# Kernel optimization log

Hardware: AMD Instinct MI355X
Metric: run time of the kernel (lower is better)

Reference implementation:

```python
import jax, jax.numpy as jnp
import numpy as np

N = 131072        # total nodes (2048 graphs * MAX_N)
E = 1048576       # edges
F_IN = 128        # g_feature_n
INT_D = 256       # int_d
H1, C1 = 8, 8     # gl: heads, head_d
C2 = 256          # gl2: out channels, heads=1
MAX_N = 64
NEG_SLOPE = 0.2
BN_EPS = 1e-5


def _gat_conv(x, src, dst, W, att_src, att_dst, bias, heads, out_c):
    """PyG GATConv (concat=True), self-loops already appended to src/dst."""
    n = x.shape[0]
    h = (x @ W.T).reshape(n, heads, out_c)                  # [N,H,C]
    a_s = jnp.sum(h * att_src, axis=-1)                     # [N,H]
    a_d = jnp.sum(h * att_dst, axis=-1)                     # [N,H]
    alpha = jax.nn.leaky_relu(a_s[src] + a_d[dst], NEG_SLOPE)  # [E',H]
    amax = jax.ops.segment_max(alpha, dst, num_segments=n)  # stable segment softmax
    e = jnp.exp(alpha - amax[dst])
    denom = jax.ops.segment_sum(e, dst, num_segments=n)
    w = e / (denom[dst] + 1e-16)                            # [E',H]
    out = jax.ops.segment_sum(h[src] * w[..., None], dst, num_segments=n)
    return out.reshape(n, heads * out_c) + bias


def setup_inputs() -> dict:
    key = jax.random.key(0)
    ks = jax.random.split(key, 20)
    s = 0.1
    return {
        "x": jax.random.normal(ks[0], (N, F_IN), jnp.float32),
        "edge_index": jax.random.randint(ks[1], (2, E), 0, N, jnp.int64),
        # lin_embed
        "We": jax.random.normal(ks[2], (INT_D, F_IN), jnp.float32) * s,
        "be": jnp.zeros((INT_D,), jnp.float32),
        # batchnorm (eval mode, running stats)
        "bn_gamma": jnp.ones((INT_D,), jnp.float32),
        "bn_beta": jnp.zeros((INT_D,), jnp.float32),
        "bn_mean": jax.random.normal(ks[3], (INT_D,), jnp.float32) * 0.01,
        "bn_var": jax.random.uniform(ks[4], (INT_D,), jnp.float32, 0.5, 1.5),
        # gl: GATConv(INT_D -> C1, heads=H1)
        "W1": jax.random.normal(ks[5], (H1 * C1, INT_D), jnp.float32) * s,
        "as1": jax.random.normal(ks[6], (1, H1, C1), jnp.float32) * s,
        "ad1": jax.random.normal(ks[7], (1, H1, C1), jnp.float32) * s,
        "b1": jnp.zeros((H1 * C1,), jnp.float32),
        # gl2: GATConv(H1*C1 -> C2, heads=1)
        "W2": jax.random.normal(ks[8], (C2, H1 * C1), jnp.float32) * s,
        "as2": jax.random.normal(ks[9], (1, 1, C2), jnp.float32) * s,
        "ad2": jax.random.normal(ks[10], (1, 1, C2), jnp.float32) * s,
        "b2": jnp.zeros((C2,), jnp.float32),
        # lin_out
        "Wo": jax.random.normal(ks[11], (1, INT_D), jnp.float32) * s,
        "bo": jnp.zeros((1,), jnp.float32),
    }


def reference(x, edge_index, We, be, bn_gamma, bn_beta, bn_mean, bn_var,
              W1, as1, ad1, b1, W2, as2, ad2, b2, Wo, bo):
    n = x.shape[0]
    loops = jnp.arange(n)
    src = jnp.concatenate([edge_index[0], loops])  # add_self_loops=True (PyG default)
    dst = jnp.concatenate([edge_index[1], loops])

    h = x @ We.T + be
    h = (h - bn_mean) * jax.lax.rsqrt(bn_var + BN_EPS) * bn_gamma + bn_beta

    h = jax.nn.elu(_gat_conv(h, src, dst, W1, as1, ad1, b1, H1, C1))
    h = _gat_conv(h, src, dst, W2, as2, ad2, b2, 1, C2)

    mu = (h @ Wo.T + bo).reshape(-1, MAX_N, 1)
    return mu, jnp.zeros_like(mu)
```

## Files before the change

### kernel.cpp

```cpp
#include <hip/hip_runtime.h>
#include <hip/hip_bf16.h>

#define NN 131072
#define NE 1048576
#define INVLN2 1.44269504088896341f

typedef unsigned short u16;
typedef unsigned int u32;

__device__ __forceinline__ float bf2f(u16 u) {
  return __uint_as_float(((unsigned int)u) << 16);
}
__device__ __forceinline__ u16 f2bf(float f) {
  unsigned int u = __float_as_uint(f);
  unsigned int r = ((u >> 16) & 1u) + 0x7fffu;
  return (u16)((u + r) >> 16);
}
__device__ __forceinline__ float leakyf(float x) { return x >= 0.f ? x : 0.2f * x; }

constexpr size_t OFF_H1   = 0;
constexpr size_t OFF_AS1N = 16777216;
constexpr size_t OFF_AD1N = 20971520;
constexpr size_t OFF_ZS   = 25165824;
constexpr size_t OFF_AD2N = 26214400;
constexpr size_t OFF_RP   = 26738688;
constexpr size_t OFF_WOFF = 27264000;
constexpr size_t OFF_COL  = 27788288;
constexpr size_t OFF_MP   = 31982592;
constexpr size_t OFF_C1AC = 32023552;
constexpr size_t OFF_V2   = 32023840;
constexpr size_t OFF_BSUM = 32024624;

__global__ __launch_bounds__(1024) void scanA_kernel(const int* cnt, int* rp, int* bsum) {
  __shared__ int buf[1024];
  int t = threadIdx.x;
  int i = blockIdx.x * 1024 + t;
  int v = cnt[i];
  buf[t] = v;
  __syncthreads();
  for (int off = 1; off < 1024; off <<= 1) {
    int a = (t >= off) ? buf[t - off] : 0;
    __syncthreads();
    buf[t] += a;
    __syncthreads();
  }
  rp[i] = buf[t] - v;
  if (t == 1023) bsum[blockIdx.x] = buf[t];
}
__global__ void scanB_kernel(int* bsum, int* rp) {
  __shared__ int buf[128];
  int t = threadIdx.x;
  int v = bsum[t];
  buf[t] = v;
  __syncthreads();
  for (int off = 1; off < 128; off <<= 1) {
    int a = (t >= off) ? buf[t - off] : 0;
    __syncthreads();
    buf[t] += a;
    __syncthreads();
  }
  bsum[t] = buf[t] - v;
  if (t == 127) rp[NN] = buf[127];
}
__global__ __launch_bounds__(1024) void scanC_kernel(int* rp, const int* bsum, int* wo) {
  int i = blockIdx.x * 1024 + threadIdx.x;
  int v = rp[i] + bsum[blockIdx.x];
  rp[i] = v;
  wo[i] = v;
}

__global__ __launch_bounds__(256) void count_fold_kernel(
    const int* __restrict__ ei, int* cnt, const float* W1, const float* We,
    const float* be, const float* bng, const float* bnb, const float* bnm,
    const float* bnv, const float* as1, const float* ad1, const float* W2,
    const float* as2, const float* ad2, const float* Wo, const float* b2,
    const float* bo, float* MP, float* c1ac, float* v2) {
  int b = blockIdx.x;
  int t = threadIdx.x;
  if (b < 4096) {
    int p = b & 7;
    int base = (b >> 3) * 2048;
    int dsts[8];
#pragma unroll
    for (int j = 0; j < 8; ++j) dsts[j] = ei[NE + base + t + 256 * j];
#pragma unroll
    for (int j = 0; j < 8; ++j)
      if ((dsts[j] >> 14) == p) atomicAdd(&cnt[dsts[j]], 1);
  } else if (b < 4136) {
    __shared__ float L[2][256];
    int mrow = b - 4096;
    int r0 = mrow * 2;
    int lr = t >> 7, k = t & 127;
    float sgc = bng[t] * rsqrtf(bnv[t] + 1e-5f);
#pragma unroll
    for (int q = 0; q < 2; ++q) {
      int r = r0 + q;
      float coef;
      if (r < 64) {
        coef = W1[r * 256 + t];
      } else if (r < 72) {
        int h = r - 64;
        coef = 0.f;
#pragma unroll
        for (int j = 0; j < 8; ++j) coef += as1[h * 8 + j] * W1[(h * 8 + j) * 256 + t];
        coef *= INVLN2;
      } else {
        int h = r - 72;
        coef = 0.f;
#pragma unroll
        for (int j = 0; j < 8; ++j) coef += ad1[h * 8 + j] * W1[(h * 8 + j) * 256 + t];
        coef *= INVLN2;
      }
      L[q][t] = coef * sgc;
    }
    __syncthreads();
    float acc = 0.f;
    for (int c = 0; c < 256; ++c) acc += L[lr][c] * We[c * 128 + k];
    MP[(size_t)(r0 + lr) * 128 + k] = acc;
  } else if (b == 4136) {
    __shared__ float ofs[256];
    __shared__ float c1l[64];
    float sgc = bng[t] * rsqrtf(bnv[t] + 1e-5f);
    ofs[t] = (be[t] - bnm[t]) * sgc + bnb[t];
    __syncthreads();
    if (t < 64) {
      float a = 0.f;
      for (int c = 0; c < 256; ++c) a += W1[t * 256 + c] * ofs[c];
      c1ac[t] = a;
      c1l[t] = a;
    }
    __syncthreads();
    if (t < 8) {
      float s = 0.f;
#pragma unroll
      for (int j = 0; j < 8; ++j) s += c1l[t * 8 + j] * (as1[t * 8 + j] + ad1[t * 8 + j]);
      c1ac[64 + t] = s * INVLN2;
    }
  } else {
    __shared__ float pa[4][64], pd[4][64], pz[4][64];
    int k = t & 63, part = t >> 6;
    float a = 0.f, d = 0.f, z = 0.f;
    for (int c = part * 64; c < part * 64 + 64; ++c) {
      float w = W2[c * 64 + k];
      a += as2[c] * w;
      d += ad2[c] * w;
      z += Wo[c] * w;
    }
    pa[part][k] = a;
    pd[part][k] = d;
    pz[part][k] = z;
    __syncthreads();
    if (t < 64) {
      v2[t]       = (pa[0][t] + pa[1][t] + pa[2][t] + pa[3][t]) * INVLN2;
      v2[64 + t]  = (pd[0][t] + pd[1][t] + pd[2][t] + pd[3][t]) * INVLN2;
      v2[128 + t] = pz[0][t] + pz[1][t] + pz[2][t] + pz[3][t];
      float cc = b2[t] * Wo[t] + b2[64 + t] * Wo[64 + t] +
                 b2[128 + t] * Wo[128 + t] + b2[192 + t] * Wo[192 + t];
      for (int o = 1; o < 64; o <<= 1) cc += __shfl_xor(cc, o);
      if (t == 0) v2[192] = cc + bo[0];
    }
  }
}

__global__ __launch_bounds__(256) void fill_gemm_kernel(const float* __restrict__ x,
                                                        const float* __restrict__ MP,
                                                        u16* __restrict__ h1,
                                                        float* __restrict__ as1n,
                                                        float* __restrict__ ad1n,
                                                        const int* __restrict__ ei,
                                                        int* wo, int* colv) {
  __shared__ float4 sM[80 * 32];
  int b = blockIdx.x;
  int t = threadIdx.x;
  if (b >= 512) {
    int fb = b - 512;
    int p = fb & 7;
    int base = (fb >> 3) * 2048;
    int dsts[8], srcs[8];
#pragma unroll
    for (int j = 0; j < 8; ++j) {
      dsts[j] = ei[NE + base + t + 256 * j];
      srcs[j] = ei[base + t + 256 * j];
    }
#pragma unroll
    for (int j = 0; j < 8; ++j) {
      if ((dsts[j] >> 14) == p) {
        int pos = atomicAdd(&wo[dsts[j]], 1);
        colv[pos] = srcs[j];
      }
    }
    return;
  }
  int lane = t & 63, wv = t >> 6;
  const float4* MPv = (const float4*)MP;
  for (int i = t; i < 2560; i += 256) sM[i] = MPv[i];
  __syncthreads();
  int c0 = (wv & 1) * 40;
  size_t r0 = (size_t)b * 256 + (wv >> 1) * 128 + lane;
  const float4* x0 = (const float4*)(x + r0 * 128);
  const float4* x1 = (const float4*)(x + (r0 + 64) * 128);
  float a0[40], a1[40];
#pragma unroll
  for (int c = 0; c < 40; ++c) { a0[c] = 0.f; a1[c] = 0.f; }
  for (int q = 0; q < 32; ++q) {
    float4 cx0 = x0[q];
    float4 cx1 = x1[q];
    const float4* mp = sM + c0 * 32 + q;
#pragma unroll
    for (int c = 0; c < 40; ++c) {
      float4 B = mp[c * 32];
      a0[c] += cx0.x * B.x; a0[c] += cx0.y * B.y;
      a0[c] += cx0.z * B.z; a0[c] += cx0.w * B.w;
      a1[c] += cx1.x * B.x; a1[c] += cx1.y * B.y;
      a1[c] += cx1.z * B.z; a1[c] += cx1.w * B.w;
    }
  }
#pragma unroll
  for (int rr = 0; rr < 2; ++rr) {
    size_t row = r0 + rr * 64;
    if (c0 == 0) {
      u32 ux[20];
#pragma unroll
      for (int j = 0; j < 20; ++j) {
        float lo = rr ? a1[2 * j] : a0[2 * j];
        float hi = rr ? a1[2 * j + 1] : a0[2 * j + 1];
        ux[j] = (u32)f2bf(lo) | ((u32)f2bf(hi) << 16);
      }
      uint4* dst = (uint4*)(h1 + row * 64);
#pragma unroll
      for (int j = 0; j < 5; ++j)
        dst[j] = make_uint4(ux[4 * j], ux[4 * j + 1], ux[4 * j + 2], ux[4 * j + 3]);
    } else {
      u32 ux[12];
#pragma unroll
      for (int j = 0; j < 12; ++j) {
        float lo = rr ? a1[2 * j] : a0[2 * j];
        float hi = rr ? a1[2 * j + 1] : a0[2 * j + 1];
        ux[j] = (u32)f2bf(lo) | ((u32)f2bf(hi) << 16);
      }
      uint4* dst = (uint4*)(h1 + row * 64 + 40);
#pragma unroll
      for (int j = 0; j < 3; ++j)
        dst[j] = make_uint4(ux[4 * j], ux[4 * j + 1], ux[4 * j + 2], ux[4 * j + 3]);
      float4* as4 = (float4*)(as1n + row * 8);
      float4* ad4 = (float4*)(ad1n + row * 8);
      if (rr == 0) {
        as4[0] = make_float4(a0[24], a0[25], a0[26], a0[27]);
        as4[1] = make_float4(a0[28], a0[29], a0[30], a0[31]);
        ad4[0] = make_float4(a0[32], a0[33], a0[34], a0[35]);
        ad4[1] = make_float4(a0[36], a0[37], a0[38], a0[39]);
      } else {
        as4[0] = make_float4(a1[24], a1[25], a1[26], a1[27]);
        as4[1] = make_float4(a1[28], a1[29], a1[30], a1[31]);
        ad4[0] = make_float4(a1[32], a1[33], a1[34], a1[35]);
        ad4[1] = make_float4(a1[36], a1[37], a1[38], a1[39]);
      }
    }
  }
}

__global__ __launch_bounds__(256) void gat1_agg_kernel(const int* __restrict__ rp,
                                                       const int* __restrict__ colv,
                                                       const float* __restrict__ as1n,
                                                       const float* __restrict__ ad1n,
                                                       const u16* __restrict__ h1,
                                                       const float* b1,
                                                       const float* __restrict__ c1ac,
                                                       const float* v2,
                                                       float2* zs, float* ad2n) {
  __shared__ float wlds[4][64];
  __shared__ int slds[4][8];
  int t = threadIdx.x, lane = t & 63, wv = t >> 6;
  int n = blockIdx.x * 4 + wv;
  int m = lane & 31;
  int half = lane >> 5;
  int hh = m >> 2;
  int h1i = lane & 7;
  int e8 = lane >> 3;
  int start = rp[n], end = rp[n + 1];
  const char* h1b = (const char*)h1;
  float adh = ad1n[(size_t)n * 8 + hh] + c1ac[64 + hh];
  float ws = exp2f(leakyf(as1n[(size_t)n * 8 + hh] + adh));
  float denom = ws;
  u32 sv = *(const u32*)(h1b + ((size_t)n << 7) + m * 4);
  float wsel = half ? 0.f : ws;
  float acc0 = wsel * __uint_as_float(sv << 16);
  float acc1 = wsel * __uint_as_float(sv & 0xffff0000u);
  float ad_p1 = ad1n[(size_t)n * 8 + h1i] + c1ac[64 + h1i];
  for (int base = start; base < end; base += 8) {
    int mm = end - base;
    if (mm > 8) mm = 8;
    int eidx = base + e8;
    int ecl = (eidx < end) ? eidx : (end - 1);
    int s = colv[ecl];
    float w = (e8 < mm) ? exp2f(leakyf(as1n[(size_t)s * 8 + h1i] + ad_p1)) : 0.f;
    if (h1i == 0) slds[wv][e8] = s;
    wlds[wv][lane] = w;
    float dsum = w;
    dsum += __shfl_xor(dsum, 8);
    dsum += __shfl_xor(dsum, 16);
    dsum += __shfl_xor(dsum, 32);
    denom += __shfl(dsum, hh);
#pragma unroll
    for (int i = 0; i < 4; ++i) {
      int e = 2 * i + half;
      float wi = wlds[wv][e * 8 + hh];
      int si = slds[wv][e];
      u32 v = *(const u32*)(h1b + ((size_t)si << 7) + m * 4);
      acc0 += wi * __uint_as_float(v << 16);
      acc1 += wi * __uint_as_float(v & 0xffff0000u);
    }
  }
  acc0 += __shfl_xor(acc0, 32);
  acc1 += __shfl_xor(acc1, 32);
  float dinv = __builtin_amdgcn_rcpf(denom + 1e-16f);
  float2 c1p = ((const float2*)c1ac)[m];
  float2 b1p = ((const float2*)b1)[m];
  float v0 = acc0 * dinv + c1p.x + b1p.x;
  float v1 = acc1 * dinv + c1p.y + b1p.y;
  v0 = v0 > 0.f ? v0 : __expf(v0) - 1.f;
  v1 = v1 > 0.f ? v1 : __expf(v1) - 1.f;
  float2 vap = ((const float2*)v2)[m];
  float2 vdp = ((const float2*)(v2 + 64))[m];
  float2 vzp = ((const float2*)(v2 + 128))[m];
  float p0 = v0 * vap.x + v1 * vap.y;
  float p1 = v0 * vdp.x + v1 * vdp.y;
  float p2 = v0 * vzp.x + v1 * vzp.y;
  for (int o = 1; o < 32; o <<= 1) {
    p0 += __shfl_xor(p0, o);
    p1 += __shfl_xor(p1, o);
    p2 += __shfl_xor(p2, o);
  }
  if (lane == 0) {
    zs[n] = make_float2(p0, p2);
    ad2n[n] = p1;
  }
}

__global__ __launch_bounds__(256) void gat2_kernel(const int* __restrict__ rp,
                                                   const int* __restrict__ colv,
                                                   const float2* __restrict__ zs,
                                                   const float* __restrict__ ad2n,
                                                   const float* v2, float* out) {
  int t = threadIdx.x;
  int g = t & 7;
  int n = blockIdx.x * 32 + (t >> 3);
  int start = rp[n], end = rp[n + 1];
  float ad = ad2n[n];
  float num = 0.f, den = 0.f;
  for (int e = start + g; e < end; e += 8) {
    int s = colv[e];
    float2 tt = zs[s];
    float wi = exp2f(leakyf(tt.x + ad));
    num += wi * tt.y;
    den += wi;
  }
  if (g == 0) {
    float2 self = zs[n];
    float w = exp2f(leakyf(self.x + ad));
    num += w * self.y;
    den += w;
  }
  num += __shfl_xor(num, 1); den += __shfl_xor(den, 1);
  num += __shfl_xor(num, 2); den += __shfl_xor(den, 2);
  num += __shfl_xor(num, 4); den += __shfl_xor(den, 4);
  if (g == 0) {
    out[n] = num * __builtin_amdgcn_rcpf(den + 1e-16f) + v2[192];
    out[NN + n] = 0.f;
  }
}

extern "C" void kernel_launch(void* const* d_in, const int* in_sizes, int n_in,
                              void* d_out, int out_size, void* d_ws, size_t ws_size,
                              hipStream_t stream) {
  const float* x   = (const float*)d_in[0];
  const int*   ei  = (const int*)d_in[1];
  const float* We  = (const float*)d_in[2];
  const float* be  = (const float*)d_in[3];
  const float* bng = (const float*)d_in[4];
  const float* bnb = (const float*)d_in[5];
  const float* bnm = (const float*)d_in[6];
  const float* bnv = (const float*)d_in[7];
  const float* W1  = (const float*)d_in[8];
  const float* as1 = (const float*)d_in[9];
  const float* ad1 = (const float*)d_in[10];
  const float* b1  = (const float*)d_in[11];
  const float* W2  = (const float*)d_in[12];
  const float* as2 = (const float*)d_in[13];
  const float* ad2 = (const float*)d_in[14];
  const float* b2  = (const float*)d_in[15];
  const float* Wo  = (const float*)d_in[16];
  const float* bo  = (const float*)d_in[17];
  float* out = (float*)d_out;

  char* ws = (char*)d_ws;
  u16*    h1   = (u16*)(ws + OFF_H1);
  float*  as1n = (float*)(ws + OFF_AS1N);
  float*  ad1n = (float*)(ws + OFF_AD1N);
  float2* zs   = (float2*)(ws + OFF_ZS);
  float*  ad2n = (float*)(ws + OFF_AD2N);
  int*    rp   = (int*)(ws + OFF_RP);
  int*    wo   = (int*)(ws + OFF_WOFF);
  int*    colv = (int*)(ws + OFF_COL);
  float*  MP   = (float*)(ws + OFF_MP);
  float*  c1ac = (float*)(ws + OFF_C1AC);
  float*  v2   = (float*)(ws + OFF_V2);
  int*    bsum = (int*)(ws + OFF_BSUM);

  hipMemsetAsync(wo, 0, NN * sizeof(int), stream);
  count_fold_kernel<<<4138, 256, 0, stream>>>(ei, wo, W1, We, be, bng, bnb, bnm, bnv,
                                              as1, ad1, W2, as2, ad2, Wo, b2, bo,
                                              MP, c1ac, v2);
  scanA_kernel<<<NN / 1024, 1024, 0, stream>>>(wo, rp, bsum);
  scanB_kernel<<<1, 128, 0, stream>>>(bsum, rp);
  scanC_kernel<<<NN / 1024, 1024, 0, stream>>>(rp, bsum, wo);
  fill_gemm_kernel<<<4608, 256, 0, stream>>>(x, MP, h1, as1n, ad1n, ei, wo, colv);
  gat1_agg_kernel<<<NN / 4, 256, 0, stream>>>(rp, colv, as1n, ad1n, h1, b1, c1ac, v2, zs, ad2n);
  gat2_kernel<<<NN / 32, 256, 0, stream>>>(rp, colv, zs, ad2n, v2, out);
}
```

Measured before the change: 214.9 us.

## Replace CSR count/scan build with fixed-capacity per-node adjacency slots

Drops the separate degree-count pass and the three-kernel prefix scan. Each node now gets a fixed block of 48 neighbor slots, filled with one atomicAdd on a per-node counter. The edge fill is split between the weight-folding kernel and the GEMM kernel, half the edges each. The aggregation kernels index slots as n*CAP and use the count as the length. gat1 also accumulates the softmax denominator per lane and does one final shuffle, instead of a shuffle reduction every 8-edge chunk. In exchange, any node with in-degree above 48 silently overwrites its neighbor's slots, and the adjacency buffer is larger and sparser.

```diff
diff --git a/kernel.cpp b/kernel.cpp
--- a/kernel.cpp
+++ b/kernel.cpp
@@ -3,6 +3,7 @@
 
 #define NN 131072
 #define NE 1048576
+#define CAP 48
 #define INVLN2 1.44269504088896341f
 
 typedef unsigned short u16;
@@ -23,72 +24,39 @@
 constexpr size_t OFF_AD1N = 20971520;
 constexpr size_t OFF_ZS   = 25165824;
 constexpr size_t OFF_AD2N = 26214400;
-constexpr size_t OFF_RP   = 26738688;
-constexpr size_t OFF_WOFF = 27264000;
-constexpr size_t OFF_COL  = 27788288;
-constexpr size_t OFF_MP   = 31982592;
-constexpr size_t OFF_C1AC = 32023552;
-constexpr size_t OFF_V2   = 32023840;
-constexpr size_t OFF_BSUM = 32024624;
-
-__global__ __launch_bounds__(1024) void scanA_kernel(const int* cnt, int* rp, int* bsum) {
-  __shared__ int buf[1024];
-  int t = threadIdx.x;
-  int i = blockIdx.x * 1024 + t;
-  int v = cnt[i];
-  buf[t] = v;
-  __syncthreads();
-  for (int off = 1; off < 1024; off <<= 1) {
-    int a = (t >= off) ? buf[t - off] : 0;
-    __syncthreads();
-    buf[t] += a;
-    __syncthreads();
-  }
-  rp[i] = buf[t] - v;
-  if (t == 1023) bsum[blockIdx.x] = buf[t];
-}
-__global__ void scanB_kernel(int* bsum, int* rp) {
-  __shared__ int buf[128];
-  int t = threadIdx.x;
-  int v = bsum[t];
-  buf[t] = v;
-  __syncthreads();
-  for (int off = 1; off < 128; off <<= 1) {
-    int a = (t >= off) ? buf[t - off] : 0;
-    __syncthreads();
-    buf[t] += a;
-    __syncthreads();
-  }
-  bsum[t] = buf[t] - v;
-  if (t == 127) rp[NN] = buf[127];
-}
-__global__ __launch_bounds__(1024) void scanC_kernel(int* rp, const int* bsum, int* wo) {
-  int i = blockIdx.x * 1024 + threadIdx.x;
-  int v = rp[i] + bsum[blockIdx.x];
-  rp[i] = v;
-  wo[i] = v;
-}
-
-__global__ __launch_bounds__(256) void count_fold_kernel(
-    const int* __restrict__ ei, int* cnt, const float* W1, const float* We,
+constexpr size_t OFF_CNT  = 26738688;
+constexpr size_t OFF_COL  = 27262976;
+constexpr size_t OFF_MP   = 52428800;
+constexpr size_t OFF_C1AC = 52469760;
+constexpr size_t OFF_V2   = 52470064;
+
+__global__ __launch_bounds__(256) void fill1_fold_kernel(
+    const int* __restrict__ ei, int* cnt, int* colv, const float* W1, const float* We,
     const float* be, const float* bng, const float* bnb, const float* bnm,
     const float* bnv, const float* as1, const float* ad1, const float* W2,
     const float* as2, const float* ad2, const float* Wo, const float* b2,
     const float* bo, float* MP, float* c1ac, float* v2) {
   int b = blockIdx.x;
   int t = threadIdx.x;
-  if (b < 4096) {
+  if (b < 2048) {
     int p = b & 7;
     int base = (b >> 3) * 2048;
-    int dsts[8];
-#pragma unroll
-    for (int j = 0; j < 8; ++j) dsts[j] = ei[NE + base + t + 256 * j];
-#pragma unroll
-    for (int j = 0; j < 8; ++j)
-      if ((dsts[j] >> 14) == p) atomicAdd(&cnt[dsts[j]], 1);
-  } else if (b < 4136) {
+    int dsts[8], srcs[8];
+#pragma unroll
+    for (int j = 0; j < 8; ++j) {
+      dsts[j] = ei[NE + base + t + 256 * j];
+      srcs[j] = ei[base + t + 256 * j];
+    }
+#pragma unroll
+    for (int j = 0; j < 8; ++j) {
+      if ((dsts[j] >> 14) == p) {
+        int slot = atomicAdd(&cnt[dsts[j]], 1);
+        colv[dsts[j] * CAP + slot] = srcs[j];
+      }
+    }
+  } else if (b < 2088) {
     __shared__ float L[2][256];
-    int mrow = b - 4096;
+    int mrow = b - 2048;
     int r0 = mrow * 2;
     int lr = t >> 7, k = t & 127;
     float sgc = bng[t] * rsqrtf(bnv[t] + 1e-5f);
@@ -117,7 +85,7 @@
     float acc = 0.f;
     for (int c = 0; c < 256; ++c) acc += L[lr][c] * We[c * 128 + k];
     MP[(size_t)(r0 + lr) * 128 + k] = acc;
-  } else if (b == 4136) {
+  } else if (b == 2088) {
     __shared__ float ofs[256];
     __shared__ float c1l[64];
     float sgc = bng[t] * rsqrtf(bnv[t] + 1e-5f);
@@ -162,20 +130,20 @@
   }
 }
 
-__global__ __launch_bounds__(256) void fill_gemm_kernel(const float* __restrict__ x,
-                                                        const float* __restrict__ MP,
-                                                        u16* __restrict__ h1,
-                                                        float* __restrict__ as1n,
-                                                        float* __restrict__ ad1n,
-                                                        const int* __restrict__ ei,
-                                                        int* wo, int* colv) {
+__global__ __launch_bounds__(256) void gemm_fill2_kernel(const float* __restrict__ x,
+                                                         const float* __restrict__ MP,
+                                                         u16* __restrict__ h1,
+                                                         float* __restrict__ as1n,
+                                                         float* __restrict__ ad1n,
+                                                         const int* __restrict__ ei,
+                                                         int* cnt, int* colv) {
   __shared__ float4 sM[80 * 32];
   int b = blockIdx.x;
   int t = threadIdx.x;
   if (b >= 512) {
     int fb = b - 512;
     int p = fb & 7;
-    int base = (fb >> 3) * 2048;
+    int base = NE / 2 + (fb >> 3) * 2048;
     int dsts[8], srcs[8];
 #pragma unroll
     for (int j = 0; j < 8; ++j) {
@@ -185,8 +153,8 @@
 #pragma unroll
     for (int j = 0; j < 8; ++j) {
       if ((dsts[j] >> 14) == p) {
-        int pos = atomicAdd(&wo[dsts[j]], 1);
-        colv[pos] = srcs[j];
+        int slot = atomicAdd(&cnt[dsts[j]], 1);
+        colv[dsts[j] * CAP + slot] = srcs[j];
       }
     }
     return;
@@ -259,7 +227,7 @@
   }
 }
 
-__global__ __launch_bounds__(256) void gat1_agg_kernel(const int* __restrict__ rp,
+__global__ __launch_bounds__(256) void gat1_agg_kernel(const int* __restrict__ cnt,
                                                        const int* __restrict__ colv,
                                                        const float* __restrict__ as1n,
                                                        const float* __restrict__ ad1n,
@@ -277,15 +245,16 @@
   int hh = m >> 2;
   int h1i = lane & 7;
   int e8 = lane >> 3;
-  int start = rp[n], end = rp[n + 1];
+  int start = n * CAP;
+  int end = start + cnt[n];
   const char* h1b = (const char*)h1;
   float adh = ad1n[(size_t)n * 8 + hh] + c1ac[64 + hh];
   float ws = exp2f(leakyf(as1n[(size_t)n * 8 + hh] + adh));
-  float denom = ws;
   u32 sv = *(const u32*)(h1b + ((size_t)n << 7) + m * 4);
   float wsel = half ? 0.f : ws;
   float acc0 = wsel * __uint_as_float(sv << 16);
   float acc1 = wsel * __uint_as_float(sv & 0xffff0000u);
+  float dd = 0.f;
   float ad_p1 = ad1n[(size_t)n * 8 + h1i] + c1ac[64 + h1i];
   for (int base = start; base < end; base += 8) {
     int mm = end - base;
@@ -296,23 +265,21 @@
     float w = (e8 < mm) ? exp2f(leakyf(as1n[(size_t)s * 8 + h1i] + ad_p1)) : 0.f;
     if (h1i == 0) slds[wv][e8] = s;
     wlds[wv][lane] = w;
-    float dsum = w;
-    dsum += __shfl_xor(dsum, 8);
-    dsum += __shfl_xor(dsum, 16);
-    dsum += __shfl_xor(dsum, 32);
-    denom += __shfl(dsum, hh);
 #pragma unroll
     for (int i = 0; i < 4; ++i) {
       int e = 2 * i + half;
       float wi = wlds[wv][e * 8 + hh];
       int si = slds[wv][e];
       u32 v = *(const u32*)(h1b + ((size_t)si << 7) + m * 4);
+      dd += wi;
       acc0 += wi * __uint_as_float(v << 16);
       acc1 += wi * __uint_as_float(v & 0xffff0000u);
     }
   }
   acc0 += __shfl_xor(acc0, 32);
   acc1 += __shfl_xor(acc1, 32);
+  dd += __shfl_xor(dd, 32);
+  float denom = ws + dd;
   float dinv = __builtin_amdgcn_rcpf(denom + 1e-16f);
   float2 c1p = ((const float2*)c1ac)[m];
   float2 b1p = ((const float2*)b1)[m];
@@ -337,7 +304,7 @@
   }
 }
 
-__global__ __launch_bounds__(256) void gat2_kernel(const int* __restrict__ rp,
+__global__ __launch_bounds__(256) void gat2_kernel(const int* __restrict__ cnt,
                                                    const int* __restrict__ colv,
                                                    const float2* __restrict__ zs,
                                                    const float* __restrict__ ad2n,
@@ -345,7 +312,8 @@
   int t = threadIdx.x;
   int g = t & 7;
   int n = blockIdx.x * 32 + (t >> 3);
-  int start = rp[n], end = rp[n + 1];
+  int start = n * CAP;
+  int end = start + cnt[n];
   float ad = ad2n[n];
   float num = 0.f, den = 0.f;
   for (int e = start + g; e < end; e += 8) {
@@ -399,22 +367,17 @@
   float*  ad1n = (float*)(ws + OFF_AD1N);
   float2* zs   = (float2*)(ws + OFF_ZS);
   float*  ad2n = (float*)(ws + OFF_AD2N);
-  int*    rp   = (int*)(ws + OFF_RP);
-  int*    wo   = (int*)(ws + OFF_WOFF);
+  int*    cnt  = (int*)(ws + OFF_CNT);
   int*    colv = (int*)(ws + OFF_COL);
   float*  MP   = (float*)(ws + OFF_MP);
   float*  c1ac = (float*)(ws + OFF_C1AC);
   float*  v2   = (float*)(ws + OFF_V2);
-  int*    bsum = (int*)(ws + OFF_BSUM);
-
-  hipMemsetAsync(wo, 0, NN * sizeof(int), stream);
-  count_fold_kernel<<<4138, 256, 0, stream>>>(ei, wo, W1, We, be, bng, bnb, bnm, bnv,
-                                              as1, ad1, W2, as2, ad2, Wo, b2, bo,
-                                              MP, c1ac, v2);
-  scanA_kernel<<<NN / 1024, 1024, 0, stream>>>(wo, rp, bsum);
-  scanB_kernel<<<1, 128, 0, stream>>>(bsum, rp);
-  scanC_kernel<<<NN / 1024, 1024, 0, stream>>>(rp, bsum, wo);
-  fill_gemm_kernel<<<4608, 256, 0, stream>>>(x, MP, h1, as1n, ad1n, ei, wo, colv);
-  gat1_agg_kernel<<<NN / 4, 256, 0, stream>>>(rp, colv, as1n, ad1n, h1, b1, c1ac, v2, zs, ad2n);
-  gat2_kernel<<<NN / 32, 256, 0, stream>>>(rp, colv, zs, ad2n, v2, out);
-}
+
+  hipMemsetAsync(cnt, 0, NN * sizeof(int), stream);
+  fill1_fold_kernel<<<2090, 256, 0, stream>>>(ei, cnt, colv, W1, We, be, bng, bnb,
+                                              bnm, bnv, as1, ad1, W2, as2, ad2, Wo,
+                                              b2, bo, MP, c1ac, v2);
+  gemm_fill2_kernel<<<2560, 256, 0, stream>>>(x, MP, h1, as1n, ad1n, ei, cnt, colv);
+  gat1_agg_kernel<<<NN / 4, 256, 0, stream>>>(cnt, colv, as1n, ad1n, h1, b1, c1ac, v2, zs, ad2n);
+  gat2_kernel<<<NN / 32, 256, 0, stream>>>(cnt, colv, zs, ad2n, v2, out);
+}
```

Result: faster. 187.3 us, median of 2 (-12.8%).
